# Kernel tuning notes

Hardware: AMD Instinct MI355X
Metric: run time of the kernel (lower is better)

Reference implementation:

```python
import jax, jax.numpy as jnp
import numpy as np

N_NODES = 50000
N_EDGES = 800000
NFEAT = 512
NHID = 128
NCLASS = 40


def setup_inputs() -> dict:
    key = jax.random.key(0)
    ks = jax.random.split(key, 12)
    s = lambda fan_in: 1.0 / np.sqrt(fan_in)
    return {
        "x": jax.random.normal(ks[0], (N_NODES, NFEAT), dtype=jnp.float32),
        "edge_src": jax.random.randint(ks[1], (N_EDGES,), 0, N_NODES, dtype=jnp.int32),
        "edge_dst": jax.random.randint(ks[2], (N_EDGES,), 0, N_NODES, dtype=jnp.int32),
        "edge_val": jax.random.uniform(ks[3], (N_EDGES,), dtype=jnp.float32) * 0.1,
        # GraphConvolution 1: nfeat -> nhid
        "W1": jax.random.uniform(ks[4], (NFEAT, NHID), jnp.float32, -s(NFEAT), s(NFEAT)),
        "b1": jnp.zeros((NHID,), jnp.float32),
        # res1 Linear: nfeat -> nhid (stored as [in, out])
        "Wr1": jax.random.uniform(ks[5], (NFEAT, NHID), jnp.float32, -s(NFEAT), s(NFEAT)),
        "br1": jnp.zeros((NHID,), jnp.float32),
        # GraphConvolution 2: 2*nhid -> nclass
        "W2": jax.random.uniform(ks[6], (2 * NHID, NCLASS), jnp.float32, -s(2 * NHID), s(2 * NHID)),
        "b2": jnp.zeros((NCLASS,), jnp.float32),
        # res2 Linear: 2*nhid -> nclass
        "Wr2": jax.random.uniform(ks[7], (2 * NHID, NCLASS), jnp.float32, -s(2 * NHID), s(2 * NHID)),
        "br2": jnp.zeros((NCLASS,), jnp.float32),
    }


def _spmm(edge_src, edge_dst, edge_val, support):
    # adj @ support with adj in COO form: out[d] += val * support[s]
    msgs = edge_val[:, None] * support[edge_src]  # [E, F] irregular gather
    return jax.ops.segment_sum(msgs, edge_dst, num_segments=N_NODES)


def reference(x, edge_src, edge_dst, edge_val, W1, b1, Wr1, br1, W2, b2, Wr2, br2):
    # gc1(x, adj) = adj @ (x @ W1) + b1
    gc1 = _spmm(edge_src, edge_dst, edge_val, x @ W1) + b1
    h = jnp.concatenate([jax.nn.relu(gc1), x @ Wr1 + br1], axis=1)  # [N, 2*nhid]
    # dropout is identity in eval mode
    gc2 = _spmm(edge_src, edge_dst, edge_val, h @ W2) + b2
    h2 = gc2 + (h @ Wr2 + br2)
    return jax.nn.log_softmax(h2, axis=1)
```

## Files before the change

### kernel.cpp

```cpp
#include <hip/hip_runtime.h>
#include <stdint.h>

#define N_NODES 50000
#define N_EDGES 800000
#define NFEAT 512
#define NHID 128
#define NCLASS 40
#define NB 196

typedef __attribute__((ext_vector_type(8))) __bf16 bf16x8;
typedef __attribute__((ext_vector_type(4))) float f32x4;

__device__ __forceinline__ uint16_t f2b(float f) {
  uint32_t x = __float_as_uint(f);
  uint32_t r = (x + 0x7fffu + ((x >> 16) & 1u)) >> 16;
  return (uint16_t)r;
}
__device__ __forceinline__ float b2f(uint16_t u) {
  return __uint_as_float(((uint32_t)u) << 16);
}

__global__ void k_cast_x(const float* __restrict__ x, uint16_t* __restrict__ xb, int n8) {
  int i = blockIdx.x * blockDim.x + threadIdx.x;
  if (i >= n8) return;
  const float4* p = (const float4*)x + (size_t)i * 2;
  float4 a = p[0], b = p[1];
  union { uint16_t u[8]; uint4 v; } o;
  o.u[0] = f2b(a.x); o.u[1] = f2b(a.y); o.u[2] = f2b(a.z); o.u[3] = f2b(a.w);
  o.u[4] = f2b(b.x); o.u[5] = f2b(b.y); o.u[6] = f2b(b.z); o.u[7] = f2b(b.w);
  ((uint4*)xb)[i] = o.v;
}

__global__ void k_prep_w1(const float* __restrict__ W1, const float* __restrict__ Wr1,
                          uint16_t* __restrict__ WT) {
  int idx = blockIdx.x * 256 + threadIdx.x;
  if (idx >= 256 * 512) return;
  int n = idx >> 9, k = idx & 511;
  float v = (n < 128) ? W1[(size_t)k * 128 + n] : Wr1[(size_t)k * 128 + (n - 128)];
  WT[idx] = f2b(v);
}

__global__ void k_prep_w2(const float* __restrict__ W2, const float* __restrict__ Wr2,
                          uint16_t* __restrict__ WT) {
  int idx = blockIdx.x * 256 + threadIdx.x;
  if (idx >= 128 * 256) return;
  int n = idx >> 8, k = idx & 255;
  float v = 0.f;
  if (n < 40) v = W2[(size_t)k * 40 + n];
  else if (n < 80) v = Wr2[(size_t)k * 40 + (n - 40)];
  WT[idx] = f2b(v);
}

__global__ void k_hist(const int* __restrict__ dst, int* __restrict__ counts) {
  int e = blockIdx.x * 256 + threadIdx.x;
  if (e < N_EDGES) atomicAdd(&counts[dst[e]], 1);
}

__global__ void k_blocksum(const int* __restrict__ counts, int* __restrict__ blocksums) {
  __shared__ int red[256];
  int t = threadIdx.x, idx = blockIdx.x * 256 + t;
  red[t] = (idx < N_NODES) ? counts[idx] : 0;
  __syncthreads();
  for (int o = 128; o; o >>= 1) {
    if (t < o) red[t] += red[t + o];
    __syncthreads();
  }
  if (t == 0) blocksums[blockIdx.x] = red[0];
}

__global__ void k_scan2(const int* __restrict__ counts, const int* __restrict__ blocksums,
                        int* __restrict__ offs) {
  __shared__ int red[256];
  __shared__ int sc[256];
  int b = blockIdx.x, t = threadIdx.x;
  red[t] = (t < b && t < NB) ? blocksums[t] : 0;
  __syncthreads();
  for (int o = 128; o; o >>= 1) {
    if (t < o) red[t] += red[t + o];
    __syncthreads();
  }
  int prefix = red[0];
  int idx = b * 256 + t;
  int c = (idx < N_NODES) ? counts[idx] : 0;
  sc[t] = c;
  __syncthreads();
  for (int o = 1; o < 256; o <<= 1) {
    int v = (t >= o) ? sc[t - o] : 0;
    __syncthreads();
    sc[t] += v;
    __syncthreads();
  }
  if (idx <= N_NODES) offs[idx] = prefix + sc[t] - c;
}

__global__ void k_scatter(const int* __restrict__ src, const int* __restrict__ dst,
                          const float* __restrict__ val, const int* __restrict__ offs,
                          int* __restrict__ cursor, int2* __restrict__ es) {
  int e = blockIdx.x * 256 + threadIdx.x;
  if (e >= N_EDGES) return;
  int d = dst[e];
  int pos = offs[d] + atomicAdd(&cursor[d], 1);
  es[pos] = make_int2(src[e], __float_as_int(val[e]));
}

__global__ __launch_bounds__(256, 2) void k_gemm1(
    const uint16_t* __restrict__ A, const uint16_t* __restrict__ BT, int M,
    uint16_t* __restrict__ S1b, uint16_t* __restrict__ h, const float* __restrict__ br1) {
  __shared__ uint16_t Al[128 * 64];
  __shared__ uint16_t Bl[128 * 64];
  const int tid = threadIdx.x;
  const int w = tid >> 6, lane = tid & 63;
  const int wm = w >> 1, wn = w & 1;
  const int m0 = blockIdx.x * 128;
  const int n0 = blockIdx.y * 128;
  const int K = NFEAT;

  f32x4 acc[4][4];
#pragma unroll
  for (int t = 0; t < 4; t++)
#pragma unroll
    for (int u = 0; u < 4; u++) acc[t][u] = (f32x4)0.f;

  const int lrow = lane >> 3;
  const int lcol = lane & 7;

  for (int kb = 0; kb < K / 64; ++kb) {
    __syncthreads();
    const int k0 = kb * 64;
#pragma unroll
    for (int i = 0; i < 4; i++) {
      int rr = (w * 4 + i) * 8 + lrow;
      int ra = m0 + rr;
      if (ra >= M) ra = M - 1;
      const uint16_t* gA = A + (size_t)ra * K + k0 + lcol * 8;
      __builtin_amdgcn_global_load_lds(
          (const __attribute__((address_space(1))) void*)gA,
          (__attribute__((address_space(3))) void*)&Al[(w * 4 + i) * 512], 16, 0, 0);
      int rb = n0 + rr;
      const uint16_t* gB = BT + (size_t)rb * K + k0 + lcol * 8;
      __builtin_amdgcn_global_load_lds(
          (const __attribute__((address_space(1))) void*)gB,
          (__attribute__((address_space(3))) void*)&Bl[(w * 4 + i) * 512], 16, 0, 0);
    }
    __syncthreads();
#pragma unroll
    for (int s = 0; s < 2; s++) {
      bf16x8 av[4], bv[4];
#pragma unroll
      for (int t = 0; t < 4; t++)
        av[t] = *(const bf16x8*)&Al[(wm * 64 + t * 16 + (lane & 15)) * 64 + s * 32 + (lane >> 4) * 8];
#pragma unroll
      for (int u = 0; u < 4; u++)
        bv[u] = *(const bf16x8*)&Bl[(wn * 64 + u * 16 + (lane & 15)) * 64 + s * 32 + (lane >> 4) * 8];
#pragma unroll
      for (int t = 0; t < 4; t++)
#pragma unroll
        for (int u = 0; u < 4; u++)
          acc[t][u] = __builtin_amdgcn_mfma_f32_16x16x32_bf16(av[t], bv[u], acc[t][u], 0, 0, 0);
    }
  }

  const int cl = lane & 15, rq = lane >> 4;
#pragma unroll
  for (int t = 0; t < 4; t++) {
#pragma unroll
    for (int u = 0; u < 4; u++) {
#pragma unroll
      for (int r = 0; r < 4; r++) {
        int m = m0 + wm * 64 + t * 16 + rq * 4 + r;
        int n = n0 + wn * 64 + u * 16 + cl;
        if (m >= M) continue;
        float v = acc[t][u][r];
        if (n < 128)
          S1b[(size_t)m * 128 + n] = f2b(v);
        else
          h[(size_t)m * 256 + n] = f2b(v + br1[n - 128]);
      }
    }
  }
}

__global__ __launch_bounds__(256, 2) void k_gemm2(
    const uint16_t* __restrict__ A, const uint16_t* __restrict__ BT, int M,
    uint16_t* __restrict__ S2b, float* __restrict__ oacc,
    const float* __restrict__ b2, const float* __restrict__ br2) {
  __shared__ uint16_t Al[128 * 64];
  __shared__ uint16_t Bl[128 * 64];
  const int tid = threadIdx.x;
  const int w = tid >> 6, lane = tid & 63;
  const int wm = w >> 1, wn = w & 1;
  const int m0 = blockIdx.x * 128;
  const int K = 256;

  f32x4 acc[4][4];
#pragma unroll
  for (int t = 0; t < 4; t++)
#pragma unroll
    for (int u = 0; u < 4; u++) acc[t][u] = (f32x4)0.f;

  const int lrow = lane >> 3;
  const int lcol = lane & 7;

  for (int kb = 0; kb < K / 64; ++kb) {
    __syncthreads();
    const int k0 = kb * 64;
#pragma unroll
    for (int i = 0; i < 4; i++) {
      int rr = (w * 4 + i) * 8 + lrow;
      int ra = m0 + rr;
      if (ra >= M) ra = M - 1;
      const uint16_t* gA = A + (size_t)ra * K + k0 + lcol * 8;
      __builtin_amdgcn_global_load_lds(
          (const __attribute__((address_space(1))) void*)gA,
          (__attribute__((address_space(3))) void*)&Al[(w * 4 + i) * 512], 16, 0, 0);
      const uint16_t* gB = BT + (size_t)rr * K + k0 + lcol * 8;
      __builtin_amdgcn_global_load_lds(
          (const __attribute__((address_space(1))) void*)gB,
          (__attribute__((address_space(3))) void*)&Bl[(w * 4 + i) * 512], 16, 0, 0);
    }
    __syncthreads();
#pragma unroll
    for (int s = 0; s < 2; s++) {
      bf16x8 av[4], bv[4];
#pragma unroll
      for (int t = 0; t < 4; t++)
        av[t] = *(const bf16x8*)&Al[(wm * 64 + t * 16 + (lane & 15)) * 64 + s * 32 + (lane >> 4) * 8];
#pragma unroll
      for (int u = 0; u < 4; u++)
        bv[u] = *(const bf16x8*)&Bl[(wn * 64 + u * 16 + (lane & 15)) * 64 + s * 32 + (lane >> 4) * 8];
#pragma unroll
      for (int t = 0; t < 4; t++)
#pragma unroll
        for (int u = 0; u < 4; u++)
          acc[t][u] = __builtin_amdgcn_mfma_f32_16x16x32_bf16(av[t], bv[u], acc[t][u], 0, 0, 0);
    }
  }

  const int cl = lane & 15, rq = lane >> 4;
#pragma unroll
  for (int t = 0; t < 4; t++) {
#pragma unroll
    for (int u = 0; u < 4; u++) {
#pragma unroll
      for (int r = 0; r < 4; r++) {
        int m = m0 + wm * 64 + t * 16 + rq * 4 + r;
        int n = wn * 64 + u * 16 + cl;
        if (m >= M) continue;
        float v = acc[t][u][r];
        if (n < 40) S2b[(size_t)m * 64 + n] = f2b(v);
        else if (n < 64) S2b[(size_t)m * 64 + n] = 0;
        if (n >= 40 && n < 80) oacc[(size_t)m * 64 + (n - 40)] = v + b2[n - 40] + br2[n - 40];
        else if (n >= 80 && n < 104) oacc[(size_t)m * 64 + (n - 40)] = 0.f;
      }
    }
  }
}

__global__ void k_spmm1_csr(const int* __restrict__ offs, const int2* __restrict__ es,
                            const uint16_t* __restrict__ S1b, const float* __restrict__ b1,
                            uint16_t* __restrict__ h) {
  int node = blockIdx.x * 4 + (threadIdx.x >> 6);
  if (node >= N_NODES) return;
  int lane = threadIdx.x & 63;
  int eg = lane >> 4;
  int fg = lane & 15;
  int beg = offs[node], end = offs[node + 1];
  float a[8];
#pragma unroll
  for (int j = 0; j < 8; j++) a[j] = 0.f;
  for (int p = beg; p < end; p += 4) {
    int pe = p + eg;
    bool ok = pe < end;
    int2 ev = es[ok ? pe : beg];
    float v = ok ? __int_as_float(ev.y) : 0.f;
    uint4 g = *(const uint4*)(S1b + (size_t)ev.x * 128 + fg * 8);
    a[0] += v * b2f((uint16_t)g.x); a[1] += v * b2f((uint16_t)(g.x >> 16));
    a[2] += v * b2f((uint16_t)g.y); a[3] += v * b2f((uint16_t)(g.y >> 16));
    a[4] += v * b2f((uint16_t)g.z); a[5] += v * b2f((uint16_t)(g.z >> 16));
    a[6] += v * b2f((uint16_t)g.w); a[7] += v * b2f((uint16_t)(g.w >> 16));
  }
#pragma unroll
  for (int j = 0; j < 8; j++) {
    a[j] += __shfl_xor(a[j], 16, 64);
    a[j] += __shfl_xor(a[j], 32, 64);
  }
  if (eg == 0) {
    const float4* bp = (const float4*)(b1 + fg * 8);
    float4 ba = bp[0], bb = bp[1];
    float r0 = a[0] + ba.x, r1 = a[1] + ba.y, r2 = a[2] + ba.z, r3 = a[3] + ba.w;
    float r4 = a[4] + bb.x, r5 = a[5] + bb.y, r6 = a[6] + bb.z, r7 = a[7] + bb.w;
    union { uint16_t u[8]; uint4 v; } o;
    o.u[0] = f2b(r0 > 0.f ? r0 : 0.f); o.u[1] = f2b(r1 > 0.f ? r1 : 0.f);
    o.u[2] = f2b(r2 > 0.f ? r2 : 0.f); o.u[3] = f2b(r3 > 0.f ? r3 : 0.f);
    o.u[4] = f2b(r4 > 0.f ? r4 : 0.f); o.u[5] = f2b(r5 > 0.f ? r5 : 0.f);
    o.u[6] = f2b(r6 > 0.f ? r6 : 0.f); o.u[7] = f2b(r7 > 0.f ? r7 : 0.f);
    *(uint4*)(h + (size_t)node * 256 + fg * 8) = o.v;
  }
}

__global__ void k_spmm2_lsm(const int* __restrict__ offs, const int2* __restrict__ es,
                            const uint16_t* __restrict__ S2b, const float* __restrict__ oacc,
                            float* __restrict__ out) {
  int node = blockIdx.x * 4 + (threadIdx.x >> 6);
  if (node >= N_NODES) return;
  int lane = threadIdx.x & 63;
  int eg = lane >> 3;
  int fg = lane & 7;
  int beg = offs[node], end = offs[node + 1];
  float a[8];
#pragma unroll
  for (int j = 0; j < 8; j++) a[j] = 0.f;
  for (int p = beg; p < end; p += 8) {
    int pe = p + eg;
    bool ok = pe < end;
    int2 ev = es[ok ? pe : beg];
    float v = ok ? __int_as_float(ev.y) : 0.f;
    uint4 g = *(const uint4*)(S2b + (size_t)ev.x * 64 + fg * 8);
    a[0] += v * b2f((uint16_t)g.x); a[1] += v * b2f((uint16_t)(g.x >> 16));
    a[2] += v * b2f((uint16_t)g.y); a[3] += v * b2f((uint16_t)(g.y >> 16));
    a[4] += v * b2f((uint16_t)g.z); a[5] += v * b2f((uint16_t)(g.z >> 16));
    a[6] += v * b2f((uint16_t)g.w); a[7] += v * b2f((uint16_t)(g.w >> 16));
  }
#pragma unroll
  for (int j = 0; j < 8; j++) {
    a[j] += __shfl_xor(a[j], 8, 64);
    a[j] += __shfl_xor(a[j], 16, 64);
    a[j] += __shfl_xor(a[j], 32, 64);
  }
  const float4* op = (const float4*)(oacc + (size_t)node * 64 + fg * 8);
  float4 o0 = op[0], o1 = op[1];
  float v0 = a[0] + o0.x, v1 = a[1] + o0.y, v2 = a[2] + o0.z, v3 = a[3] + o0.w;
  float v4 = a[4] + o1.x, v5 = a[5] + o1.y, v6 = a[6] + o1.z, v7 = a[7] + o1.w;
  bool valid = fg < 5;
  float m01 = v0 > v1 ? v0 : v1, m23 = v2 > v3 ? v2 : v3;
  float m45 = v4 > v5 ? v4 : v5, m67 = v6 > v7 ? v6 : v7;
  float ml = m01 > m23 ? m01 : m23;
  float mh = m45 > m67 ? m45 : m67;
  float mv = ml > mh ? ml : mh;
  mv = valid ? mv : -1e30f;
#pragma unroll
  for (int o = 1; o <= 4; o <<= 1) {
    float t = __shfl_xor(mv, o, 64);
    mv = mv > t ? mv : t;
  }
  float se = 0.f;
  if (valid)
    se = __expf(v0 - mv) + __expf(v1 - mv) + __expf(v2 - mv) + __expf(v3 - mv) +
         __expf(v4 - mv) + __expf(v5 - mv) + __expf(v6 - mv) + __expf(v7 - mv);
#pragma unroll
  for (int o = 1; o <= 4; o <<= 1) se += __shfl_xor(se, o, 64);
  if (eg == 0 && valid) {
    float ls = mv + __logf(se);
    float4 r0 = make_float4(v0 - ls, v1 - ls, v2 - ls, v3 - ls);
    float4 r1 = make_float4(v4 - ls, v5 - ls, v6 - ls, v7 - ls);
    float4* wp = (float4*)(out + (size_t)node * 40 + fg * 8);
    wp[0] = r0;
    wp[1] = r1;
  }
}

extern "C" void kernel_launch(void* const* d_in, const int* in_sizes, int n_in,
                              void* d_out, int out_size, void* d_ws, size_t ws_size,
                              hipStream_t stream) {
  const float* x = (const float*)d_in[0];
  const int* esrc = (const int*)d_in[1];
  const int* edst = (const int*)d_in[2];
  const float* eval = (const float*)d_in[3];
  const float* W1 = (const float*)d_in[4];
  const float* b1 = (const float*)d_in[5];
  const float* Wr1 = (const float*)d_in[6];
  const float* br1 = (const float*)d_in[7];
  const float* W2 = (const float*)d_in[8];
  const float* b2 = (const float*)d_in[9];
  const float* Wr2 = (const float*)d_in[10];
  const float* br2 = (const float*)d_in[11];
  float* out = (float*)d_out;

  char* ws = (char*)d_ws;
  uint16_t* xb   = (uint16_t*)(ws);
  uint16_t* S1b  = (uint16_t*)(ws + 51200000);
  uint16_t* h    = (uint16_t*)(ws + 64000000);
  uint16_t* WT1  = (uint16_t*)(ws + 89600000);
  uint16_t* WT2  = (uint16_t*)(ws + 89862144);
  uint16_t* S2b  = (uint16_t*)(ws + 89927680);
  float*    oacc = (float*)(ws + 96327680);
  int*      counts = (int*)(ws + 109127680);
  int*      cursor = (int*)(ws + 109327680);
  int*      offs   = (int*)(ws + 109527680);
  int2*     es     = (int2*)(ws + 109727696);
  int*      blocksums = (int*)(ws + 116127696);

  hipMemsetAsync(counts, 0, 400000, stream);

  k_cast_x<<<(3200000 + 255) / 256, 256, 0, stream>>>(x, xb, 3200000);
  k_prep_w1<<<(256 * 512) / 256, 256, 0, stream>>>(W1, Wr1, WT1);
  k_prep_w2<<<(128 * 256) / 256, 256, 0, stream>>>(W2, Wr2, WT2);

  k_hist<<<(N_EDGES + 255) / 256, 256, 0, stream>>>(edst, counts);
  k_blocksum<<<NB, 256, 0, stream>>>(counts, blocksums);
  k_scan2<<<NB, 256, 0, stream>>>(counts, blocksums, offs);
  k_scatter<<<(N_EDGES + 255) / 256, 256, 0, stream>>>(esrc, edst, eval, offs, cursor, es);

  dim3 g1(391, 2);
  k_gemm1<<<g1, 256, 0, stream>>>(xb, WT1, N_NODES, S1b, h, br1);

  k_spmm1_csr<<<(N_NODES + 3) / 4, 256, 0, stream>>>(offs, es, S1b, b1, h);

  k_gemm2<<<391, 256, 0, stream>>>(h, WT2, N_NODES, S2b, oacc, b2, br2);

  k_spmm2_lsm<<<(N_NODES + 3) / 4, 256, 0, stream>>>(offs, es, S2b, oacc, out);
}
```

Measured before the change: 382.5 us.

## Fuse preprocessing kernels and switch SpMM gathers to packed fp16 math

Merges the x cast, both weight-transpose preps and the edge histogram into one launch, split by block index, to cut launch overhead. Stores the gathered supports S1/S2 as fp16 instead of bf16. The SpMM kernels now accumulate with packed half2 FMAs and reduce with half2 shuffles, halving arithmetic and register use in the gather loops. This trades fp32 accumulation for fp16 accumulation, which risks accuracy loss and overflow on high-degree nodes.

```diff
diff --git a/kernel.cpp b/kernel.cpp
--- a/kernel.cpp
+++ b/kernel.cpp
@@ -10,50 +10,45 @@
 
 typedef __attribute__((ext_vector_type(8))) __bf16 bf16x8;
 typedef __attribute__((ext_vector_type(4))) float f32x4;
+typedef _Float16 h2 __attribute__((ext_vector_type(2)));
 
 __device__ __forceinline__ uint16_t f2b(float f) {
   uint32_t x = __float_as_uint(f);
   uint32_t r = (x + 0x7fffu + ((x >> 16) & 1u)) >> 16;
   return (uint16_t)r;
 }
-__device__ __forceinline__ float b2f(uint16_t u) {
-  return __uint_as_float(((uint32_t)u) << 16);
-}
-
-__global__ void k_cast_x(const float* __restrict__ x, uint16_t* __restrict__ xb, int n8) {
-  int i = blockIdx.x * blockDim.x + threadIdx.x;
-  if (i >= n8) return;
-  const float4* p = (const float4*)x + (size_t)i * 2;
-  float4 a = p[0], b = p[1];
-  union { uint16_t u[8]; uint4 v; } o;
-  o.u[0] = f2b(a.x); o.u[1] = f2b(a.y); o.u[2] = f2b(a.z); o.u[3] = f2b(a.w);
-  o.u[4] = f2b(b.x); o.u[5] = f2b(b.y); o.u[6] = f2b(b.z); o.u[7] = f2b(b.w);
-  ((uint4*)xb)[i] = o.v;
-}
-
-__global__ void k_prep_w1(const float* __restrict__ W1, const float* __restrict__ Wr1,
-                          uint16_t* __restrict__ WT) {
-  int idx = blockIdx.x * 256 + threadIdx.x;
-  if (idx >= 256 * 512) return;
-  int n = idx >> 9, k = idx & 511;
-  float v = (n < 128) ? W1[(size_t)k * 128 + n] : Wr1[(size_t)k * 128 + (n - 128)];
-  WT[idx] = f2b(v);
-}
-
-__global__ void k_prep_w2(const float* __restrict__ W2, const float* __restrict__ Wr2,
-                          uint16_t* __restrict__ WT) {
-  int idx = blockIdx.x * 256 + threadIdx.x;
-  if (idx >= 128 * 256) return;
-  int n = idx >> 8, k = idx & 255;
-  float v = 0.f;
-  if (n < 40) v = W2[(size_t)k * 40 + n];
-  else if (n < 80) v = Wr2[(size_t)k * 40 + (n - 40)];
-  WT[idx] = f2b(v);
-}
-
-__global__ void k_hist(const int* __restrict__ dst, int* __restrict__ counts) {
-  int e = blockIdx.x * 256 + threadIdx.x;
-  if (e < N_EDGES) atomicAdd(&counts[dst[e]], 1);
+
+__global__ void k_pre(const float* __restrict__ x, uint16_t* __restrict__ xb,
+                      const float* __restrict__ W1, const float* __restrict__ Wr1,
+                      uint16_t* __restrict__ WT1,
+                      const float* __restrict__ W2, const float* __restrict__ Wr2,
+                      uint16_t* __restrict__ WT2,
+                      const int* __restrict__ dst, int* __restrict__ counts) {
+  int b = blockIdx.x, tid = threadIdx.x;
+  if (b < 12500) {
+    int i = b * 256 + tid;
+    const float4* p = (const float4*)x + (size_t)i * 2;
+    float4 a = p[0], c = p[1];
+    union { uint16_t u[8]; uint4 v; } o;
+    o.u[0] = f2b(a.x); o.u[1] = f2b(a.y); o.u[2] = f2b(a.z); o.u[3] = f2b(a.w);
+    o.u[4] = f2b(c.x); o.u[5] = f2b(c.y); o.u[6] = f2b(c.z); o.u[7] = f2b(c.w);
+    ((uint4*)xb)[i] = o.v;
+  } else if (b < 13012) {
+    int idx = (b - 12500) * 256 + tid;
+    int n = idx >> 9, k = idx & 511;
+    float v = (n < 128) ? W1[(size_t)k * 128 + n] : Wr1[(size_t)k * 128 + (n - 128)];
+    WT1[idx] = f2b(v);
+  } else if (b < 13140) {
+    int idx = (b - 13012) * 256 + tid;
+    int n = idx >> 8, k = idx & 255;
+    float v = 0.f;
+    if (n < 40) v = W2[(size_t)k * 40 + n];
+    else if (n < 80) v = Wr2[(size_t)k * 40 + (n - 40)];
+    WT2[idx] = f2b(v);
+  } else {
+    int e = (b - 13140) * 256 + tid;
+    atomicAdd(&counts[dst[e]], 1);
+  }
 }
 
 __global__ void k_blocksum(const int* __restrict__ counts, int* __restrict__ blocksums) {
@@ -105,7 +100,7 @@
 
 __global__ __launch_bounds__(256, 2) void k_gemm1(
     const uint16_t* __restrict__ A, const uint16_t* __restrict__ BT, int M,
-    uint16_t* __restrict__ S1b, uint16_t* __restrict__ h, const float* __restrict__ br1) {
+    _Float16* __restrict__ S1h, uint16_t* __restrict__ h, const float* __restrict__ br1) {
   __shared__ uint16_t Al[128 * 64];
   __shared__ uint16_t Bl[128 * 64];
   const int tid = threadIdx.x;
@@ -172,7 +167,7 @@
         if (m >= M) continue;
         float v = acc[t][u][r];
         if (n < 128)
-          S1b[(size_t)m * 128 + n] = f2b(v);
+          S1h[(size_t)m * 128 + n] = (_Float16)v;
         else
           h[(size_t)m * 256 + n] = f2b(v + br1[n - 128]);
       }
@@ -182,7 +177,7 @@
 
 __global__ __launch_bounds__(256, 2) void k_gemm2(
     const uint16_t* __restrict__ A, const uint16_t* __restrict__ BT, int M,
-    uint16_t* __restrict__ S2b, float* __restrict__ oacc,
+    _Float16* __restrict__ S2h, float* __restrict__ oacc,
     const float* __restrict__ b2, const float* __restrict__ br2) {
   __shared__ uint16_t Al[128 * 64];
   __shared__ uint16_t Bl[128 * 64];
@@ -247,8 +242,8 @@
         int n = wn * 64 + u * 16 + cl;
         if (m >= M) continue;
         float v = acc[t][u][r];
-        if (n < 40) S2b[(size_t)m * 64 + n] = f2b(v);
-        else if (n < 64) S2b[(size_t)m * 64 + n] = 0;
+        if (n < 40) S2h[(size_t)m * 64 + n] = (_Float16)v;
+        else if (n < 64) S2h[(size_t)m * 64 + n] = (_Float16)0.f;
         if (n >= 40 && n < 80) oacc[(size_t)m * 64 + (n - 40)] = v + b2[n - 40] + br2[n - 40];
         else if (n >= 80 && n < 104) oacc[(size_t)m * 64 + (n - 40)] = 0.f;
       }
@@ -257,7 +252,7 @@
 }
 
 __global__ void k_spmm1_csr(const int* __restrict__ offs, const int2* __restrict__ es,
-                            const uint16_t* __restrict__ S1b, const float* __restrict__ b1,
+                            const _Float16* __restrict__ S1h, const float* __restrict__ b1,
                             uint16_t* __restrict__ h) {
   int node = blockIdx.x * 4 + (threadIdx.x >> 6);
   if (node >= N_NODES) return;
@@ -265,30 +260,35 @@
   int eg = lane >> 4;
   int fg = lane & 15;
   int beg = offs[node], end = offs[node + 1];
-  float a[8];
-#pragma unroll
-  for (int j = 0; j < 8; j++) a[j] = 0.f;
+  h2 acc[4];
+#pragma unroll
+  for (int j = 0; j < 4; j++) acc[j] = (h2)(_Float16)0.f;
   for (int p = beg; p < end; p += 4) {
     int pe = p + eg;
     bool ok = pe < end;
     int2 ev = es[ok ? pe : beg];
     float v = ok ? __int_as_float(ev.y) : 0.f;
-    uint4 g = *(const uint4*)(S1b + (size_t)ev.x * 128 + fg * 8);
-    a[0] += v * b2f((uint16_t)g.x); a[1] += v * b2f((uint16_t)(g.x >> 16));
-    a[2] += v * b2f((uint16_t)g.y); a[3] += v * b2f((uint16_t)(g.y >> 16));
-    a[4] += v * b2f((uint16_t)g.z); a[5] += v * b2f((uint16_t)(g.z >> 16));
-    a[6] += v * b2f((uint16_t)g.w); a[7] += v * b2f((uint16_t)(g.w >> 16));
-  }
-#pragma unroll
-  for (int j = 0; j < 8; j++) {
-    a[j] += __shfl_xor(a[j], 16, 64);
-    a[j] += __shfl_xor(a[j], 32, 64);
+    _Float16 vh = (_Float16)v;
+    h2 vv = {vh, vh};
+    uint4 g = *(const uint4*)(S1h + (size_t)ev.x * 128 + fg * 8);
+    h2* hp = (h2*)&g;
+#pragma unroll
+    for (int j = 0; j < 4; j++) acc[j] = vv * hp[j] + acc[j];
+  }
+#pragma unroll
+  for (int j = 0; j < 4; j++) {
+    int b16 = __shfl_xor(__builtin_bit_cast(int, acc[j]), 16, 64);
+    acc[j] = acc[j] + __builtin_bit_cast(h2, b16);
+    int b32 = __shfl_xor(__builtin_bit_cast(int, acc[j]), 32, 64);
+    acc[j] = acc[j] + __builtin_bit_cast(h2, b32);
   }
   if (eg == 0) {
     const float4* bp = (const float4*)(b1 + fg * 8);
     float4 ba = bp[0], bb = bp[1];
-    float r0 = a[0] + ba.x, r1 = a[1] + ba.y, r2 = a[2] + ba.z, r3 = a[3] + ba.w;
-    float r4 = a[4] + bb.x, r5 = a[5] + bb.y, r6 = a[6] + bb.z, r7 = a[7] + bb.w;
+    float r0 = (float)acc[0][0] + ba.x, r1 = (float)acc[0][1] + ba.y;
+    float r2 = (float)acc[1][0] + ba.z, r3 = (float)acc[1][1] + ba.w;
+    float r4 = (float)acc[2][0] + bb.x, r5 = (float)acc[2][1] + bb.y;
+    float r6 = (float)acc[3][0] + bb.z, r7 = (float)acc[3][1] + bb.w;
     union { uint16_t u[8]; uint4 v; } o;
     o.u[0] = f2b(r0 > 0.f ? r0 : 0.f); o.u[1] = f2b(r1 > 0.f ? r1 : 0.f);
     o.u[2] = f2b(r2 > 0.f ? r2 : 0.f); o.u[3] = f2b(r3 > 0.f ? r3 : 0.f);
@@ -299,7 +299,7 @@
 }
 
 __global__ void k_spmm2_lsm(const int* __restrict__ offs, const int2* __restrict__ es,
-                            const uint16_t* __restrict__ S2b, const float* __restrict__ oacc,
+                            const _Float16* __restrict__ S2h, const float* __restrict__ oacc,
                             float* __restrict__ out) {
   int node = blockIdx.x * 4 + (threadIdx.x >> 6);
   if (node >= N_NODES) return;
@@ -307,30 +307,36 @@
   int eg = lane >> 3;
   int fg = lane & 7;
   int beg = offs[node], end = offs[node + 1];
-  float a[8];
-#pragma unroll
-  for (int j = 0; j < 8; j++) a[j] = 0.f;
+  h2 acc[4];
+#pragma unroll
+  for (int j = 0; j < 4; j++) acc[j] = (h2)(_Float16)0.f;
   for (int p = beg; p < end; p += 8) {
     int pe = p + eg;
     bool ok = pe < end;
     int2 ev = es[ok ? pe : beg];
     float v = ok ? __int_as_float(ev.y) : 0.f;
-    uint4 g = *(const uint4*)(S2b + (size_t)ev.x * 64 + fg * 8);
-    a[0] += v * b2f((uint16_t)g.x); a[1] += v * b2f((uint16_t)(g.x >> 16));
-    a[2] += v * b2f((uint16_t)g.y); a[3] += v * b2f((uint16_t)(g.y >> 16));
-    a[4] += v * b2f((uint16_t)g.z); a[5] += v * b2f((uint16_t)(g.z >> 16));
-    a[6] += v * b2f((uint16_t)g.w); a[7] += v * b2f((uint16_t)(g.w >> 16));
-  }
-#pragma unroll
-  for (int j = 0; j < 8; j++) {
-    a[j] += __shfl_xor(a[j], 8, 64);
-    a[j] += __shfl_xor(a[j], 16, 64);
-    a[j] += __shfl_xor(a[j], 32, 64);
+    _Float16 vh = (_Float16)v;
+    h2 vv = {vh, vh};
+    uint4 g = *(const uint4*)(S2h + (size_t)ev.x * 64 + fg * 8);
+    h2* hp = (h2*)&g;
+#pragma unroll
+    for (int j = 0; j < 4; j++) acc[j] = vv * hp[j] + acc[j];
+  }
+#pragma unroll
+  for (int j = 0; j < 4; j++) {
+    int b8 = __shfl_xor(__builtin_bit_cast(int, acc[j]), 8, 64);
+    acc[j] = acc[j] + __builtin_bit_cast(h2, b8);
+    int b16 = __shfl_xor(__builtin_bit_cast(int, acc[j]), 16, 64);
+    acc[j] = acc[j] + __builtin_bit_cast(h2, b16);
+    int b32 = __shfl_xor(__builtin_bit_cast(int, acc[j]), 32, 64);
+    acc[j] = acc[j] + __builtin_bit_cast(h2, b32);
   }
   const float4* op = (const float4*)(oacc + (size_t)node * 64 + fg * 8);
   float4 o0 = op[0], o1 = op[1];
-  float v0 = a[0] + o0.x, v1 = a[1] + o0.y, v2 = a[2] + o0.z, v3 = a[3] + o0.w;
-  float v4 = a[4] + o1.x, v5 = a[5] + o1.y, v6 = a[6] + o1.z, v7 = a[7] + o1.w;
+  float v0 = (float)acc[0][0] + o0.x, v1 = (float)acc[0][1] + o0.y;
+  float v2 = (float)acc[1][0] + o0.z, v3 = (float)acc[1][1] + o0.w;
+  float v4 = (float)acc[2][0] + o1.x, v5 = (float)acc[2][1] + o1.y;
+  float v6 = (float)acc[3][0] + o1.z, v7 = (float)acc[3][1] + o1.w;
   bool valid = fg < 5;
   float m01 = v0 > v1 ? v0 : v1, m23 = v2 > v3 ? v2 : v3;
   float m45 = v4 > v5 ? v4 : v5, m67 = v6 > v7 ? v6 : v7;
@@ -378,11 +384,11 @@
 
   char* ws = (char*)d_ws;
   uint16_t* xb   = (uint16_t*)(ws);
-  uint16_t* S1b  = (uint16_t*)(ws + 51200000);
+  _Float16* S1h  = (_Float16*)(ws + 51200000);
   uint16_t* h    = (uint16_t*)(ws + 64000000);
   uint16_t* WT1  = (uint16_t*)(ws + 89600000);
   uint16_t* WT2  = (uint16_t*)(ws + 89862144);
-  uint16_t* S2b  = (uint16_t*)(ws + 89927680);
+  _Float16* S2h  = (_Float16*)(ws + 89927680);
   float*    oacc = (float*)(ws + 96327680);
   int*      counts = (int*)(ws + 109127680);
   int*      cursor = (int*)(ws + 109327680);
@@ -392,21 +398,18 @@
 
   hipMemsetAsync(counts, 0, 400000, stream);
 
-  k_cast_x<<<(3200000 + 255) / 256, 256, 0, stream>>>(x, xb, 3200000);
-  k_prep_w1<<<(256 * 512) / 256, 256, 0, stream>>>(W1, Wr1, WT1);
-  k_prep_w2<<<(128 * 256) / 256, 256, 0, stream>>>(W2, Wr2, WT2);
-
-  k_hist<<<(N_EDGES + 255) / 256, 256, 0, stream>>>(edst, counts);
+  k_pre<<<16265, 256, 0, stream>>>(x, xb, W1, Wr1, WT1, W2, Wr2, WT2, edst, counts);
+
   k_blocksum<<<NB, 256, 0, stream>>>(counts, blocksums);
   k_scan2<<<NB, 256, 0, stream>>>(counts, blocksums, offs);
   k_scatter<<<(N_EDGES + 255) / 256, 256, 0, stream>>>(esrc, edst, eval, offs, cursor, es);
 
   dim3 g1(391, 2);
-  k_gemm1<<<g1, 256, 0, stream>>>(xb, WT1, N_NODES, S1b, h, br1);
-
-  k_spmm1_csr<<<(N_NODES + 3) / 4, 256, 0, stream>>>(offs, es, S1b, b1, h);
-
-  k_gemm2<<<391, 256, 0, stream>>>(h, WT2, N_NODES, S2b, oacc, b2, br2);
-
-  k_spmm2_lsm<<<(N_NODES + 3) / 4, 256, 0, stream>>>(offs, es, S2b, oacc, out);
-}
+  k_gemm1<<<g1, 256, 0, stream>>>(xb, WT1, N_NODES, S1h, h, br1);
+
+  k_spmm1_csr<<<(N_NODES + 3) / 4, 256, 0, stream>>>(offs, es, S1h, b1, h);
+
+  k_gemm2<<<391, 256, 0, stream>>>(h, WT2, N_NODES, S2h, oacc, b2, br2);
+
+  k_spmm2_lsm<<<(N_NODES + 3) / 4, 256, 0, stream>>>(offs, es, S2h, oacc, out);
+}
```

Measured after the change: 366.7 us. 1.04x faster.
